# Kernel tuning notes

Measured on AMD Instinct MI355X. Metric: run time of the kernel, lower is better.

Reference implementation:

```python
import jax, jax.numpy as jnp
import numpy as np

HIDDEN = 2048
NUM_HEADS = 32
NUM_KV_HEADS = 8
HEAD_DIM = HIDDEN // NUM_HEADS  # 64
GROUP = NUM_HEADS // NUM_KV_HEADS  # 4
B, S = 2, 2048


def setup_inputs() -> dict:
    key = jax.random.key(0)
    ks = jax.random.split(key, 9)
    sc = 0.02
    kv_dim = NUM_KV_HEADS * HEAD_DIM
    return {
        "x": jax.random.normal(ks[0], (B, S, HIDDEN), jnp.float32),
        # weights stored as [in, out] (transpose of torch Linear.weight)
        "Wq": jax.random.normal(ks[1], (HIDDEN, HIDDEN), jnp.float32) * sc,
        "bq": jnp.zeros((HIDDEN,), jnp.float32),
        "Wk": jax.random.normal(ks[2], (HIDDEN, kv_dim), jnp.float32) * sc,
        "bk": jnp.zeros((kv_dim,), jnp.float32),
        "Wv": jax.random.normal(ks[3], (HIDDEN, kv_dim), jnp.float32) * sc,
        "bv": jnp.zeros((kv_dim,), jnp.float32),
        "Wo": jax.random.normal(ks[4], (HIDDEN, HIDDEN), jnp.float32) * sc,
        "bo": jnp.zeros((HIDDEN,), jnp.float32),
    }


def reference(x, Wq, bq, Wk, bk, Wv, bv, Wo, bo):
    b, s, _ = x.shape
    q = (x @ Wq + bq).reshape(b, s, NUM_KV_HEADS, GROUP, HEAD_DIM)
    k = (x @ Wk + bk).reshape(b, s, NUM_KV_HEADS, HEAD_DIM)
    v = (x @ Wv + bv).reshape(b, s, NUM_KV_HEADS, HEAD_DIM)
    scale = 1.0 / jnp.sqrt(jnp.asarray(HEAD_DIM, x.dtype))
    # scores: [b, g(kv heads), r(q per group), s(query), t(key)]
    scores = jnp.einsum("bsgrd,btgd->bgrst", q, k) * scale
    attn = jax.nn.softmax(scores, axis=-1)  # dropout rate 0 -> identity
    out = jnp.einsum("bgrst,btgd->bsgrd", attn, v).reshape(b, s, HIDDEN)
    return out @ Wo + bo
```

## Files before the change

kernel.cpp:

```cpp
#include <hip/hip_runtime.h>

#define HIDDEN 2048
#define NHEADS 32
#define NKV 8
#define HD 64
#define BATCH 2
#define SEQ 2048
#define KVD 512
#define BSZ 4096
#define QKVD 3072

typedef __bf16 bfx8 __attribute__((ext_vector_type(8)));
typedef __bf16 bfx4 __attribute__((ext_vector_type(4)));
typedef __bf16 bfx2 __attribute__((ext_vector_type(2)));
typedef float f32x4 __attribute__((ext_vector_type(4)));
typedef unsigned int ux4 __attribute__((ext_vector_type(4)));

#define QSCALE 0.1803368801111204f

__device__ __forceinline__ void gl_lds16(const __bf16* g, __bf16* l) {
    __builtin_amdgcn_global_load_lds(
        (const __attribute__((address_space(1))) unsigned int*)g,
        (__attribute__((address_space(3))) unsigned int*)l, 16, 0, 0);
}

__device__ __forceinline__ unsigned int pk2(float lo, float hi) {
    bfx2 v = {(__bf16)lo, (__bf16)hi};
    return __builtin_bit_cast(unsigned int, v);
}

__global__ __launch_bounds__(256) void cvt_bf16(const float* __restrict__ src,
                                                __bf16* __restrict__ dst, int n4) {
    int i = blockIdx.x * 256 + threadIdx.x;
    if (i >= n4) return;
    float4 f = ((const float4*)src)[i];
    bfx4 o = {(__bf16)f.x, (__bf16)f.y, (__bf16)f.z, (__bf16)f.w};
    *(bfx4*)(dst + (size_t)i * 4) = o;
}

__device__ __forceinline__ void tcvt_tile(const float* __restrict__ src,
                                          __bf16* __restrict__ dst,
                                          int R, int C, int tx, int ty,
                                          float (*tile)[65], int t, float mul) {
    int br = ty * 64, bc = tx * 64;
    {
        int r = t >> 4, c = (t & 15) * 4;
#pragma unroll
        for (int i = 0; i < 4; ++i) {
            float4 v = *(const float4*)(&src[(long)(br + r + i * 16) * C + bc + c]);
            tile[r + i * 16][c + 0] = v.x * mul;
            tile[r + i * 16][c + 1] = v.y * mul;
            tile[r + i * 16][c + 2] = v.z * mul;
            tile[r + i * 16][c + 3] = v.w * mul;
        }
    }
    __syncthreads();
    {
        int d = t >> 2, tt0 = (t & 3) * 16;
        bfx8 o0, o1;
#pragma unroll
        for (int j = 0; j < 8; ++j) o0[j] = (__bf16)tile[tt0 + j][d];
#pragma unroll
        for (int j = 0; j < 8; ++j) o1[j] = (__bf16)tile[tt0 + 8 + j][d];
        *(bfx8*)(&dst[(long)(bc + d) * R + br + tt0]) = o0;
        *(bfx8*)(&dst[(long)(bc + d) * R + br + tt0 + 8]) = o1;
    }
}

__global__ __launch_bounds__(256) void prep(const float* __restrict__ Wq,
                                            const float* __restrict__ Wk,
                                            const float* __restrict__ Wv,
                                            const float* __restrict__ Wo,
                                            const float* __restrict__ bq,
                                            const float* __restrict__ bk,
                                            const float* __restrict__ bv,
                                            __bf16* __restrict__ wqkvt,
                                            __bf16* __restrict__ wot,
                                            float* __restrict__ bqkv) {
    __shared__ float tile[64][65];
    int idx = blockIdx.x, t = threadIdx.x;
    if (idx < 1024) {
        tcvt_tile(Wq, wqkvt, HIDDEN, HIDDEN, idx & 31, idx >> 5, tile, t, QSCALE);
    } else if (idx < 1280) {
        int l = idx - 1024;
        tcvt_tile(Wk, wqkvt + (size_t)HIDDEN * HIDDEN, HIDDEN, KVD, l & 7, l >> 3, tile, t, 1.0f);
    } else if (idx < 1536) {
        int l = idx - 1280;
        tcvt_tile(Wv, wqkvt + (size_t)(HIDDEN + KVD) * HIDDEN, HIDDEN, KVD, l & 7, l >> 3, tile, t, 1.0f);
    } else if (idx < 2560) {
        int l = idx - 1536;
        tcvt_tile(Wo, wot, HIDDEN, HIDDEN, l & 31, l >> 5, tile, t, 1.0f);
    } else {
        int i = (idx - 2560) * 256 + t;
        if (i < QKVD) {
            float v = (i < HIDDEN) ? bq[i] * QSCALE
                                   : (i < HIDDEN + KVD ? bk[i - HIDDEN] : bv[i - HIDDEN - KVD]);
            bqkv[i] = v;
        }
    }
}

__global__ __launch_bounds__(256) void transpose_v(const __bf16* __restrict__ qkv,
                                                   __bf16* __restrict__ vt) {
    __shared__ __bf16 tile[64][65];
    int t = threadIdx.x;
    int nb0 = blockIdx.x * 64;
    int bh = blockIdx.y;
    int b = bh >> 3, kv = bh & 7;
    {
        int tt = t >> 2, c0 = (t & 3) * 16;
        const __bf16* p = &qkv[(long)(b * SEQ + nb0 + tt) * QKVD + HIDDEN + KVD + kv * HD + c0];
        bfx8 a0 = *(const bfx8*)(p);
        bfx8 a1 = *(const bfx8*)(p + 8);
#pragma unroll
        for (int j = 0; j < 8; ++j) tile[tt][c0 + j] = a0[j];
#pragma unroll
        for (int j = 0; j < 8; ++j) tile[tt][c0 + 8 + j] = a1[j];
    }
    __syncthreads();
    {
        int d = t >> 2, tt0 = (t & 3) * 16;
        bfx8 o0, o1;
#pragma unroll
        for (int j = 0; j < 8; ++j) o0[j] = tile[tt0 + j][d];
#pragma unroll
        for (int j = 0; j < 8; ++j) o1[j] = tile[tt0 + 8 + j][d];
        __bf16* q = &vt[((long)bh * HD + d) * SEQ + nb0 + tt0];
        *(bfx8*)(q) = o0;
        *(bfx8*)(q + 8) = o1;
    }
}

template <bool OUT_BF16>
__global__ __launch_bounds__(256, 3) void gemm128(const __bf16* __restrict__ A,
                                                  const __bf16* __restrict__ Bt,
                                                  const float* __restrict__ bias,
                                                  void* __restrict__ C,
                                                  int M, int N, int K) {
    __shared__ __align__(16) __bf16 As[2][128 * 32];
    __shared__ __align__(16) __bf16 Bs[2][128 * 32];
    int t = threadIdx.x;
    int w = t >> 6, lane = t & 63;
    int lrow = lane & 15, quad = lane >> 4;
    long m0 = (long)blockIdx.y * 128, n0 = (long)blockIdx.x * 128;
    int wr = (w >> 1) * 64, wc = (w & 1) * 64;
    f32x4 acc[4][4] = {};
    int srow = t >> 2, scol = (((t & 3) ^ ((t >> 3) & 3))) * 8;
    int sA = (lrow >> 1) & 3;
    const __bf16* Ag = A + (m0 + srow) * (long)K + scol;
    const __bf16* Bg = Bt + (n0 + srow) * (long)K + scol;
#define STAGE_G(kb, buf)                                                      \
    {                                                                         \
        _Pragma("unroll") for (int c = 0; c < 2; ++c) {                       \
            gl_lds16(Ag + (long)c * 64 * K + (kb), &As[buf][c * 2048 + w * 512]); \
            gl_lds16(Bg + (long)c * 64 * K + (kb), &Bs[buf][c * 2048 + w * 512]); \
        }                                                                     \
    }
    STAGE_G(0, 0);
    int nk = K >> 5;
    for (int it = 0; it < nk; ++it) {
        __syncthreads();
        if (it + 1 < nk) STAGE_G((it + 1) * 32, (it + 1) & 1);
        const __bf16* Ab = &As[it & 1][0];
        const __bf16* Bb = &Bs[it & 1][0];
        bfx8 af[4], bfr[4];
#pragma unroll
        for (int i = 0; i < 4; ++i)
            af[i] = *(const bfx8*)&Ab[(wr + i * 16 + lrow) * 32 + ((quad ^ sA) * 8)];
#pragma unroll
        for (int j = 0; j < 4; ++j)
            bfr[j] = *(const bfx8*)&Bb[(wc + j * 16 + lrow) * 32 + ((quad ^ sA) * 8)];
#pragma unroll
        for (int i = 0; i < 4; ++i)
#pragma unroll
            for (int j = 0; j < 4; ++j)
                acc[i][j] = __builtin_amdgcn_mfma_f32_16x16x32_bf16(af[i], bfr[j], acc[i][j], 0, 0, 0);
    }
#undef STAGE_G
#pragma unroll
    for (int j = 0; j < 4; ++j) {
        long col = n0 + wc + j * 16 + lrow;
        float bv = bias[col];
#pragma unroll
        for (int i = 0; i < 4; ++i) {
#pragma unroll
            for (int r = 0; r < 4; ++r) {
                long row = m0 + wr + i * 16 + quad * 4 + r;
                float val = acc[i][j][r] + bv;
                if (OUT_BF16)
                    ((__bf16*)C)[row * N + col] = (__bf16)val;
                else
                    ((float*)C)[row * N + col] = val;
            }
        }
    }
}

__global__ __launch_bounds__(256, 2) void attn(const __bf16* __restrict__ QKV,
                                               const __bf16* __restrict__ Vt,
                                               __bf16* __restrict__ O) {
    __shared__ __align__(16) __bf16 Ks[2][64 * 64];
    __shared__ __align__(16) __bf16 Vs[2][64 * 64];
    int t = threadIdx.x;
    int w = t >> 6, lane = t & 63;
    int lrow = lane & 15, quad = lane >> 4;
    int qb = blockIdx.x, bh = blockIdx.y;
    int b = bh >> 5, h = bh & 31, kv = h >> 2;
    int q0 = qb * 256 + w * 64;

    bfx8 qf[4][2];
#pragma unroll
    for (int i = 0; i < 4; ++i)
#pragma unroll
        for (int kk = 0; kk < 2; ++kk)
            qf[i][kk] = *(const bfx8*)(QKV + (long)(b * SEQ + q0 + i * 16 + lrow) * QKVD +
                                       h * HD + kk * 32 + quad * 8);

    int srow = t >> 2, scol = (((t & 3) ^ ((t >> 3) & 3))) * 8;
    int sA = (lrow >> 1) & 3;
    const __bf16* kg = QKV + (long)(b * SEQ + srow) * QKVD + HIDDEN + kv * HD + scol;
    const __bf16* vg = Vt + ((long)(b * NKV + kv) * HD + srow) * SEQ + scol;
#define STAGE_KV(nb, buf)                                                          \
    {                                                                              \
        _Pragma("unroll") for (int c = 0; c < 2; ++c) {                            \
            gl_lds16(kg + (long)(nb)*QKVD + c * 32, &Ks[buf][c * 2048 + w * 512]); \
            gl_lds16(vg + (nb) + c * 32, &Vs[buf][c * 2048 + w * 512]);            \
        }                                                                          \
    }
    STAGE_KV(0, 0);

    f32x4 accO[4][4] = {};
    float lacc[4] = {0.f, 0.f, 0.f, 0.f};

    for (int it = 0; it < SEQ / 64; ++it) {
        __syncthreads();
        if (it + 1 < SEQ / 64) STAGE_KV((it + 1) * 64, (it + 1) & 1);
        const __bf16* Kb = &Ks[it & 1][0];
        const __bf16* Vb = &Vs[it & 1][0];
#pragma unroll
        for (int ch = 0; ch < 2; ++ch) {
            int rcol = (quad ^ sA) * 8;
            bfx8 ka0a = *(const bfx8*)&Kb[(2 * ch + 0) * 512 + lrow * 32 + rcol];
            bfx8 ka1a = *(const bfx8*)&Kb[2048 + (2 * ch + 0) * 512 + lrow * 32 + rcol];
            bfx8 ka0b = *(const bfx8*)&Kb[(2 * ch + 1) * 512 + lrow * 32 + rcol];
            bfx8 ka1b = *(const bfx8*)&Kb[2048 + (2 * ch + 1) * 512 + lrow * 32 + rcol];
            bfx8 va[4];
#pragma unroll
            for (int dt = 0; dt < 4; ++dt)
                va[dt] = *(const bfx8*)&Vb[ch * 2048 + (dt * 16 + lrow) * 32 + rcol];
#pragma unroll
            for (int i = 0; i < 4; ++i) {
                f32x4 za = {}, zb = {};
                za = __builtin_amdgcn_mfma_f32_16x16x32_bf16(ka0a, qf[i][0], za, 0, 0, 0);
                zb = __builtin_amdgcn_mfma_f32_16x16x32_bf16(ka0b, qf[i][0], zb, 0, 0, 0);
                f32x4 sa = __builtin_amdgcn_mfma_f32_16x16x32_bf16(ka1a, qf[i][1], za, 0, 0, 0);
                f32x4 sb = __builtin_amdgcn_mfma_f32_16x16x32_bf16(ka1b, qf[i][1], zb, 0, 0, 0);
                float pa0 = __builtin_amdgcn_exp2f(sa[0]);
                float pa1 = __builtin_amdgcn_exp2f(sa[1]);
                float pa2 = __builtin_amdgcn_exp2f(sa[2]);
                float pa3 = __builtin_amdgcn_exp2f(sa[3]);
                float pb0 = __builtin_amdgcn_exp2f(sb[0]);
                float pb1 = __builtin_amdgcn_exp2f(sb[1]);
                float pb2 = __builtin_amdgcn_exp2f(sb[2]);
                float pb3 = __builtin_amdgcn_exp2f(sb[3]);
                lacc[i] += ((pa0 + pa1) + (pa2 + pa3)) + ((pb0 + pb1) + (pb2 + pb3));
                unsigned int A0 = pk2(pa0, pa1), A1 = pk2(pa2, pa3);
                unsigned int B0 = pk2(pb0, pb1), B1 = pk2(pb2, pb3);
                asm volatile("v_permlane32_swap_b32 %0, %1" : "+v"(A0), "+v"(B0));
                asm volatile("v_permlane16_swap_b32 %0, %1" : "+v"(A0), "+v"(B0));
                asm volatile("v_permlane32_swap_b32 %0, %1" : "+v"(A1), "+v"(B1));
                asm volatile("v_permlane16_swap_b32 %0, %1" : "+v"(A1), "+v"(B1));
                ux4 pw = {A0, A1, B0, B1};
                bfx8 p8 = __builtin_bit_cast(bfx8, pw);
#pragma unroll
                for (int dt = 0; dt < 4; ++dt)
                    accO[dt][i] = __builtin_amdgcn_mfma_f32_16x16x32_bf16(va[dt], p8, accO[dt][i], 0, 0, 0);
            }
        }
    }
    float inv[4];
#pragma unroll
    for (int i = 0; i < 4; ++i) {
        float l = lacc[i];
        l += __shfl_xor(l, 16);
        l += __shfl_xor(l, 32);
        inv[i] = 1.0f / l;
    }
#pragma unroll
    for (int i = 0; i < 4; ++i) {
        long row = (long)(b * SEQ + q0 + i * 16 + lrow);
#pragma unroll
        for (int dt = 0; dt < 4; ++dt) {
            bfx4 o4 = {(__bf16)(accO[dt][i][0] * inv[i]), (__bf16)(accO[dt][i][1] * inv[i]),
                       (__bf16)(accO[dt][i][2] * inv[i]), (__bf16)(accO[dt][i][3] * inv[i])};
            *(bfx4*)&O[row * HIDDEN + h * HD + dt * 16 + quad * 4] = o4;
        }
    }
#undef STAGE_KV
}

extern "C" void kernel_launch(void* const* d_in, const int* in_sizes, int n_in,
                              void* d_out, int out_size, void* d_ws, size_t ws_size,
                              hipStream_t stream) {
    const float* x  = (const float*)d_in[0];
    const float* Wq = (const float*)d_in[1];
    const float* bq = (const float*)d_in[2];
    const float* Wk = (const float*)d_in[3];
    const float* bk = (const float*)d_in[4];
    const float* Wv = (const float*)d_in[5];
    const float* bv = (const float*)d_in[6];
    const float* Wo = (const float*)d_in[7];
    const float* bo = (const float*)d_in[8];
    float* out = (float*)d_out;

    __bf16* ws    = (__bf16*)d_ws;
    __bf16* xb    = ws;
    __bf16* wqkvt = xb + (size_t)BSZ * HIDDEN;
    __bf16* wot   = wqkvt + (size_t)QKVD * HIDDEN;
    __bf16* qkv   = wot + (size_t)HIDDEN * HIDDEN;
    __bf16* vt_   = qkv + (size_t)BSZ * QKVD;
    __bf16* ab_   = vt_ + (size_t)BSZ * KVD;
    float*  bqkv  = (float*)(ab_ + (size_t)BSZ * HIDDEN);

    cvt_bf16<<<(BSZ * HIDDEN / 4 + 255) / 256, 256, 0, stream>>>(x, xb, BSZ * HIDDEN / 4);
    prep<<<2560 + (QKVD + 255) / 256, 256, 0, stream>>>(Wq, Wk, Wv, Wo, bq, bk, bv,
                                                        wqkvt, wot, bqkv);

    gemm128<true><<<dim3(QKVD / 128, BSZ / 128), 256, 0, stream>>>(xb, wqkvt, bqkv, qkv, BSZ, QKVD, HIDDEN);

    transpose_v<<<dim3(SEQ / 64, BATCH * NKV), 256, 0, stream>>>(qkv, vt_);
    attn<<<dim3(SEQ / 256, BATCH * NHEADS), 256, 0, stream>>>(qkv, vt_, ab_);

    gemm128<false><<<dim3(HIDDEN / 128, BSZ / 128), 256, 0, stream>>>(ab_, wot, bo, out, BSZ, HIDDEN, HIDDEN);
}
```

Before: 318.9 us.

## Drop LDS staging in attention, load K/V directly from global with smaller tiles

The attention kernel no longer double-buffers K and V tiles through shared memory. Each wave now loads its MFMA operands directly from global memory (relying on L1/L2 cache), handles 32 query rows instead of 64, and the grid doubles to compensate. Launch bounds rise to 4 blocks per CU, and s_setprio hints are placed around the MFMA sections. This removes the barriers and LDS traffic but increases global/cache load traffic per FLOP, since K/V reuse across waves now comes only from cache.

```diff
diff --git a/kernel.cpp b/kernel.cpp
--- a/kernel.cpp
+++ b/kernel.cpp
@@ -196,65 +196,53 @@
     }
 }
 
-__global__ __launch_bounds__(256, 2) void attn(const __bf16* __restrict__ QKV,
+__global__ __launch_bounds__(256, 4) void attn(const __bf16* __restrict__ QKV,
                                                const __bf16* __restrict__ Vt,
                                                __bf16* __restrict__ O) {
-    __shared__ __align__(16) __bf16 Ks[2][64 * 64];
-    __shared__ __align__(16) __bf16 Vs[2][64 * 64];
     int t = threadIdx.x;
     int w = t >> 6, lane = t & 63;
     int lrow = lane & 15, quad = lane >> 4;
     int qb = blockIdx.x, bh = blockIdx.y;
     int b = bh >> 5, h = bh & 31, kv = h >> 2;
-    int q0 = qb * 256 + w * 64;
-
-    bfx8 qf[4][2];
-#pragma unroll
-    for (int i = 0; i < 4; ++i)
+    int q0 = qb * 128 + w * 32;
+
+    bfx8 qf[2][2];
+#pragma unroll
+    for (int i = 0; i < 2; ++i)
 #pragma unroll
         for (int kk = 0; kk < 2; ++kk)
             qf[i][kk] = *(const bfx8*)(QKV + (long)(b * SEQ + q0 + i * 16 + lrow) * QKVD +
                                        h * HD + kk * 32 + quad * 8);
 
-    int srow = t >> 2, scol = (((t & 3) ^ ((t >> 3) & 3))) * 8;
-    int sA = (lrow >> 1) & 3;
-    const __bf16* kg = QKV + (long)(b * SEQ + srow) * QKVD + HIDDEN + kv * HD + scol;
-    const __bf16* vg = Vt + ((long)(b * NKV + kv) * HD + srow) * SEQ + scol;
-#define STAGE_KV(nb, buf)                                                          \
-    {                                                                              \
-        _Pragma("unroll") for (int c = 0; c < 2; ++c) {                            \
-            gl_lds16(kg + (long)(nb)*QKVD + c * 32, &Ks[buf][c * 2048 + w * 512]); \
-            gl_lds16(vg + (nb) + c * 32, &Vs[buf][c * 2048 + w * 512]);            \
-        }                                                                          \
-    }
-    STAGE_KV(0, 0);
-
-    f32x4 accO[4][4] = {};
-    float lacc[4] = {0.f, 0.f, 0.f, 0.f};
+    const __bf16* kp0 = QKV + (long)(b * SEQ) * QKVD + HIDDEN + kv * HD + (long)lrow * QKVD + quad * 8;
+    const __bf16* vp0 = Vt + ((long)(b * NKV + kv) * HD + lrow) * SEQ + quad * 8;
+
+    f32x4 accO[4][2] = {};
+    float lacc[2] = {0.f, 0.f};
 
     for (int it = 0; it < SEQ / 64; ++it) {
-        __syncthreads();
-        if (it + 1 < SEQ / 64) STAGE_KV((it + 1) * 64, (it + 1) & 1);
-        const __bf16* Kb = &Ks[it & 1][0];
-        const __bf16* Vb = &Vs[it & 1][0];
 #pragma unroll
         for (int ch = 0; ch < 2; ++ch) {
-            int rcol = (quad ^ sA) * 8;
-            bfx8 ka0a = *(const bfx8*)&Kb[(2 * ch + 0) * 512 + lrow * 32 + rcol];
-            bfx8 ka1a = *(const bfx8*)&Kb[2048 + (2 * ch + 0) * 512 + lrow * 32 + rcol];
-            bfx8 ka0b = *(const bfx8*)&Kb[(2 * ch + 1) * 512 + lrow * 32 + rcol];
-            bfx8 ka1b = *(const bfx8*)&Kb[2048 + (2 * ch + 1) * 512 + lrow * 32 + rcol];
+            int kbase = it * 64 + ch * 32;
+            const __bf16* kp = kp0 + (long)kbase * QKVD;
+            bfx8 ka0a = *(const bfx8*)(kp);
+            bfx8 ka1a = *(const bfx8*)(kp + 32);
+            bfx8 ka0b = *(const bfx8*)(kp + (long)16 * QKVD);
+            bfx8 ka1b = *(const bfx8*)(kp + (long)16 * QKVD + 32);
+            const __bf16* vp = vp0 + kbase;
             bfx8 va[4];
 #pragma unroll
             for (int dt = 0; dt < 4; ++dt)
-                va[dt] = *(const bfx8*)&Vb[ch * 2048 + (dt * 16 + lrow) * 32 + rcol];
-#pragma unroll
-            for (int i = 0; i < 4; ++i) {
+                va[dt] = *(const bfx8*)(vp + (long)dt * 16 * SEQ);
+#pragma unroll
+            for (int i = 0; i < 2; ++i) {
+                __builtin_amdgcn_s_setprio(1);
                 f32x4 za = {}, zb = {};
                 za = __builtin_amdgcn_mfma_f32_16x16x32_bf16(ka0a, qf[i][0], za, 0, 0, 0);
                 zb = __builtin_amdgcn_mfma_f32_16x16x32_bf16(ka0b, qf[i][0], zb, 0, 0, 0);
                 f32x4 sa = __builtin_amdgcn_mfma_f32_16x16x32_bf16(ka1a, qf[i][1], za, 0, 0, 0);
                 f32x4 sb = __builtin_amdgcn_mfma_f32_16x16x32_bf16(ka1b, qf[i][1], zb, 0, 0, 0);
+                __builtin_amdgcn_s_setprio(0);
                 float pa0 = __builtin_amdgcn_exp2f(sa[0]);
                 float pa1 = __builtin_amdgcn_exp2f(sa[1]);
                 float pa2 = __builtin_amdgcn_exp2f(sa[2]);
@@ -272,22 +260,24 @@
                 asm volatile("v_permlane16_swap_b32 %0, %1" : "+v"(A1), "+v"(B1));
                 ux4 pw = {A0, A1, B0, B1};
                 bfx8 p8 = __builtin_bit_cast(bfx8, pw);
+                __builtin_amdgcn_s_setprio(1);
 #pragma unroll
                 for (int dt = 0; dt < 4; ++dt)
                     accO[dt][i] = __builtin_amdgcn_mfma_f32_16x16x32_bf16(va[dt], p8, accO[dt][i], 0, 0, 0);
+                __builtin_amdgcn_s_setprio(0);
             }
         }
     }
-    float inv[4];
-#pragma unroll
-    for (int i = 0; i < 4; ++i) {
+    float inv[2];
+#pragma unroll
+    for (int i = 0; i < 2; ++i) {
         float l = lacc[i];
         l += __shfl_xor(l, 16);
         l += __shfl_xor(l, 32);
         inv[i] = 1.0f / l;
     }
 #pragma unroll
-    for (int i = 0; i < 4; ++i) {
+    for (int i = 0; i < 2; ++i) {
         long row = (long)(b * SEQ + q0 + i * 16 + lrow);
 #pragma unroll
         for (int dt = 0; dt < 4; ++dt) {
@@ -296,7 +286,6 @@
             *(bfx4*)&O[row * HIDDEN + h * HD + dt * 16 + quad * 4] = o4;
         }
     }
-#undef STAGE_KV
 }
 
 extern "C" void kernel_launch(void* const* d_in, const int* in_sizes, int n_in,
@@ -329,7 +318,7 @@
     gemm128<true><<<dim3(QKVD / 128, BSZ / 128), 256, 0, stream>>>(xb, wqkvt, bqkv, qkv, BSZ, QKVD, HIDDEN);
 
     transpose_v<<<dim3(SEQ / 64, BATCH * NKV), 256, 0, stream>>>(qkv, vt_);
-    attn<<<dim3(SEQ / 256, BATCH * NHEADS), 256, 0, stream>>>(qkv, vt_, ab_);
+    attn<<<dim3(SEQ / 128, BATCH * NHEADS), 256, 0, stream>>>(qkv, vt_, ab_);
 
     gemm128<false><<<dim3(HIDDEN / 128, BSZ / 128), 256, 0, stream>>>(ab_, wot, bo, out, BSZ, HIDDEN, HIDDEN);
 }
```

Result: slower. 465.0 us (+45.8%).
